# Performance work log

Hardware: AMD Instinct MI355X
Metric: run time of the kernel (lower is better)

Reference implementation:

```python
import jax, jax.numpy as jnp
import numpy as np

B, C, HH, WW, HEADS = 4, 64, 256, 256, 8
CH = C // HEADS              # 8 per-head dim
HID = int(C * 2.66)          # 170
EPS_LN = 1e-5
EPS = 1e-6
QK_NORM = 1.0
# crpe windows for 8 heads: {3:2, 5:3, 7:3}; each conv input split = head_split*Ch*2
WINDOWS = [(3, 2), (5, 3), (7, 3)]


def conv2d(x, w, b=None, groups=1, pad=0):
    out = jax.lax.conv_general_dilated(
        x, w, (1, 1), [(pad, pad), (pad, pad)],
        dimension_numbers=('NCHW', 'OIHW', 'NCHW'), feature_group_count=groups)
    return out if b is None else out + b[None, :, None, None]


def setup_inputs() -> dict:
    key = jax.random.key(0)
    ks = jax.random.split(key, 32)
    p = lambda k, shp, s=0.05: jax.random.normal(k, shp, jnp.float32) * s
    inp = {
        'x': jax.random.normal(ks[0], (B, HH * WW, C), jnp.float32),
        'ln1_w': jnp.ones((C,), jnp.float32) + p(ks[1], (C,), 0.01),
        'sca_w': p(ks[2], (C, C, 1, 1)), 'sca_b': p(ks[3], (C,)),
        'dw1_w': p(ks[4], (2 * C, C, 1, 1)),          # 1x1 dim->2dim
        'dw2_w': p(ks[5], (C, 2, 3, 3)),              # grouped 3x3, groups=C, in/grp=2
        'qkv_w': p(ks[6], (3 * C, C, 1, 1)),
        'qkv_dw_w': p(ks[7], (3 * C, 1, 3, 3)),       # depthwise 3x3
        'temperature': jnp.ones((HEADS, 1, 1), jnp.float32),
        'r3_w': p(ks[8], (2, 2 * CH, 3, 3)), 'r3_b': p(ks[9], (2,)),
        'r5_w': p(ks[10], (3, 2 * CH, 5, 5)), 'r5_b': p(ks[11], (3,)),
        'r7_w': p(ks[12], (3, 2 * CH, 7, 7)), 'r7_b': p(ks[13], (3,)),
        'proj_w': p(ks[14], (C, C, 1, 1)),
        'ln2_w': jnp.ones((C,), jnp.float32) + p(ks[15], (C,), 0.01),
        'pin_w': p(ks[16], (2 * HID, C, 1, 1)),
        'ffn_dw_w': p(ks[17], (2 * HID, 1, 3, 3)),
        'pout_w': p(ks[18], (C, HID, 1, 1)),
        'H': HH, 'W': WW,
    }
    return inp


def biasfree_ln(x, w):
    # BiasFree LayerNorm over channel dim of NCHW (var only, no mean-subtract)
    sigma = jnp.var(x, axis=1, keepdims=True)
    return x / jnp.sqrt(sigma + EPS_LN) * w[None, :, None, None]


def refine_att(q, k, H, W, convs):
    # q: (B,h,N,Ch)  k: (B,h,Ch,N) -> per-head conv relative position map (B,h,N,1)
    b, h, N, Ch = q.shape
    q_img = q.transpose(0, 1, 3, 2).reshape(b, h, Ch, H, W)
    k_img = k.reshape(b, h, Ch, H, W)
    qk = jnp.concatenate([q_img, k_img], axis=2).reshape(b, h * 2 * Ch, H, W)
    splits = np.cumsum([s * 2 * Ch for _, s in WINDOWS])[:-1]
    parts = jnp.split(qk, splits, axis=1)
    outs = [conv2d(xp, wt, bs, groups=g, pad=win // 2)
            for (win, g), (wt, bs), xp in zip(WINDOWS, convs, parts)]
    att = jnp.concatenate(outs, axis=1)           # (b, h, H, W)
    return att.reshape(b, h, 1, H * W).transpose(0, 1, 3, 2)  # (b,h,N,1)


def attention(x, sca_w, sca_b, dw1_w, dw2_w, qkv_w, qkv_dw_w, temperature,
              refine_convs, proj_w, H, W):
    b, c, _, _ = x.shape
    N = H * W
    xsca = conv2d(jnp.mean(x, axis=(2, 3), keepdims=True), sca_w, sca_b)
    x1 = conv2d(conv2d(x, dw1_w), dw2_w, groups=c, pad=1)
    qkv = conv2d(conv2d(x, qkv_w), qkv_dw_w, groups=3 * c, pad=1)
    q, k, v = jnp.split(qkv, 3, axis=1)
    q = q.reshape(b, HEADS, CH, N).transpose(0, 1, 3, 2)  # b h N Ch
    k = k.reshape(b, HEADS, CH, N)                        # b h Ch N
    v = v.reshape(b, HEADS, CH, N).transpose(0, 1, 3, 2)  # b h N Ch
    q = q / (jnp.linalg.norm(q, axis=-1, keepdims=True) / QK_NORM + EPS)
    k = k / (jnp.linalg.norm(k, axis=-2, keepdims=True) / QK_NORM + EPS)
    refine_w = jax.nn.sigmoid(refine_att(q, k, H, W, refine_convs))
    attn = k @ v                                           # b h Ch Ch
    out_num = jnp.sum(v, axis=-2, keepdims=True) + q @ attn
    ksum = jnp.sum(k, axis=-1, keepdims=True)              # b h Ch 1
    out_den = jnp.asarray(N, q.dtype) + q @ ksum + EPS     # b h N 1 (bcast to Ch)
    out = out_num / out_den * temperature
    out = out * refine_w
    out = out.transpose(0, 1, 3, 2).reshape(b, c, H, W)
    out = out * xsca * jax.nn.gelu(x1, approximate=False)
    return conv2d(out, proj_w)


def feedforward(x, pin_w, ffn_dw_w, pout_w):
    h = conv2d(x, pin_w)
    h = conv2d(h, ffn_dw_w, groups=2 * HID, pad=1)
    h1, h2 = jnp.split(h, 2, axis=1)
    return conv2d(jax.nn.gelu(h1, approximate=False) * h2, pout_w)


def reference(x, ln1_w, sca_w, sca_b, dw1_w, dw2_w, qkv_w, qkv_dw_w, temperature,
              r3_w, r3_b, r5_w, r5_b, r7_w, r7_b, proj_w, ln2_w,
              pin_w, ffn_dw_w, pout_w, H, W):
    b = x.shape[0]
    xi = x.reshape(b, H, W, C).transpose(0, 3, 1, 2)  # NCHW
    refine_convs = [(r3_w, r3_b), (r5_w, r5_b), (r7_w, r7_b)]
    xi = xi + attention(biasfree_ln(xi, ln1_w), sca_w, sca_b, dw1_w, dw2_w,
                        qkv_w, qkv_dw_w, temperature, refine_convs, proj_w, H, W)
    xi = xi + feedforward(biasfree_ln(xi, ln2_w), pin_w, ffn_dw_w, pout_w)
    return xi
```

## Files before the change

### kernel.cpp

```cpp
#include <hip/hip_runtime.h>
#include <math.h>
#include <stdio.h>

#define BB 4
#define NP 65536

typedef unsigned short u16;
typedef unsigned int u32;
typedef __attribute__((ext_vector_type(8))) short short8;
typedef __attribute__((ext_vector_type(4))) float f32x4;
typedef __attribute__((ext_vector_type(2))) float f32x2;

__device__ __forceinline__ float bf2f(u16 u) { return __uint_as_float((u32)u << 16); }
__device__ __forceinline__ u16 f2bf(float f) {
  u32 u = __float_as_uint(f);
  u = (u + 0x7FFFu + ((u >> 16) & 1u)) >> 16;
  return (u16)u;
}
__device__ __forceinline__ float gelu_f(float x) {
  return 0.5f * x * (1.f + erff(x * 0.70710678118654752f));
}
__device__ __forceinline__ float wlo(u32 w) { return __uint_as_float(w << 16); }
__device__ __forceinline__ float whi(u32 w) { return __uint_as_float(w & 0xFFFF0000u); }

__global__ __launch_bounds__(256) void k_trans_stats(const float* __restrict__ x,
                                                     float* __restrict__ xi,
                                                     u16* __restrict__ xb1,
                                                     float* __restrict__ meanraw) {
  __shared__ float tile[64 * 65];
  __shared__ float s1a[64], s2a[64], sig[64], cm[64];
  int b = blockIdx.y;
  long n0 = (long)blockIdx.x * 64;
  int t = threadIdx.x;
  for (int i = t; i < 4096; i += 256) {
    int nl = i >> 6, c = i & 63;
    tile[nl * 65 + c] = x[((long)b * NP + n0 + nl) * 64 + c];
  }
  if (t < 64) { s1a[t] = 0.f; s2a[t] = 0.f; cm[t] = 0.f; }
  __syncthreads();
  {
    int nl = t & 63, part = t >> 6;
    float p1 = 0.f, p2 = 0.f;
    for (int cc = 0; cc < 16; cc++) {
      float v = tile[nl * 65 + part * 16 + cc];
      p1 += v; p2 += v * v;
    }
    atomicAdd(&s1a[nl], p1); atomicAdd(&s2a[nl], p2);
  }
  __syncthreads();
  if (t < 64) {
    float m = s1a[t] * (1.f / 64.f);
    float var = s2a[t] * (1.f / 64.f) - m * m;
    sig[t] = rsqrtf(var + 1e-5f);
  }
  __syncthreads();
  int nl = t & 63;
  int part = t >> 6;
  float sgv = sig[nl];
  for (int j = 0; j < 16; j++) {
    int i = t + 256 * j;
    int c = i >> 6;
    float v = tile[nl * 65 + c];
    xi[((long)b * 64 + c) * NP + n0 + nl] = v;
    float a = v * sgv;
    for (int off = 32; off; off >>= 1) a += __shfl_down(a, off);
    if ((t & 63) == 0) atomicAdd(&cm[c], a);
  }
  {
    u16* rp = xb1 + ((long)b * NP + n0 + nl) * 64 + part * 16;
    uint4 pk[2];
    u32 tmp[8];
#pragma unroll
    for (int g = 0; g < 2; g++) {
#pragma unroll
      for (int e = 0; e < 4; e++) {
        float v0 = tile[nl * 65 + part * 16 + g * 8 + 2 * e] * sgv;
        float v1 = tile[nl * 65 + part * 16 + g * 8 + 2 * e + 1] * sgv;
        tmp[e] = (u32)f2bf(v0) | ((u32)f2bf(v1) << 16);
      }
      pk[g].x = tmp[0]; pk[g].y = tmp[1]; pk[g].z = tmp[2]; pk[g].w = tmp[3];
      *(uint4*)(rp + g * 8) = pk[g];
    }
  }
  __syncthreads();
  if (t < 64) atomicAdd(&meanraw[b * 64 + t], cm[t]);
}

__global__ void k_xsca(const float* __restrict__ meanraw, const float* __restrict__ lnw,
                       const float* __restrict__ sca_w, const float* __restrict__ sca_b,
                       float* __restrict__ xsca) {
  int t = threadIdx.x;
  int b = t >> 6, co = t & 63;
  float a = sca_b[co];
  for (int ci = 0; ci < 64; ci++)
    a += sca_w[co * 64 + ci] * meanraw[b * 64 + ci] * lnw[ci] * (1.f / 65536.f);
  xsca[t] = a;
}

__global__ void k_foldW1b(const float* __restrict__ qkv_w, const float* __restrict__ dw1_w,
                          const float* __restrict__ lnw, u16* __restrict__ W1b) {
  int i = blockIdx.x * 256 + threadIdx.x;
  if (i < 320 * 64) {
    int co = i >> 6, ci = i & 63;
    float w = (co < 192) ? qkv_w[co * 64 + ci] : dw1_w[(co - 192) * 64 + ci];
    W1b[i] = f2bf(w * lnw[ci]);
  }
}
__global__ void k_foldW2b(const float* __restrict__ pin_w, const float* __restrict__ lnw,
                          u16* __restrict__ W2b) {
  int i = blockIdx.x * 256 + threadIdx.x;
  if (i < 384 * 64) {
    int co = i >> 6, ci = i & 63;
    float v = 0.f;
    if (co < 340) {
      int pair = co >> 1, which = co & 1;
      v = pin_w[(pair + which * 170) * 64 + ci] * lnw[ci];
    }
    W2b[i] = f2bf(v);
  }
}
__global__ void k_foldWpb(const float* __restrict__ w, u16* __restrict__ Wpb) {
  int i = blockIdx.x * 256 + threadIdx.x;
  if (i < 4096) Wpb[i] = f2bf(w[i]);
}
__global__ void k_tpoutb(const float* __restrict__ w, u16* __restrict__ Wob) {
  int i = blockIdx.x * 256 + threadIdx.x;
  if (i < 64 * 192) {
    int co = i / 192, ci = i - co * 192;
    Wob[i] = (ci < 170) ? f2bf(w[co * 170 + ci]) : (u16)0;
  }
}

template <int EPI>
__global__ __launch_bounds__(256) void k_mgemm(const u16* __restrict__ in, long in_bs,
                                               const u16* __restrict__ W,
                                               u16* __restrict__ outp, long out_bs,
                                               float* __restrict__ xo,
                                               u16* __restrict__ xb2r) {
  int t = threadIdx.x;
  int lane = t & 63, wv = t >> 6;
  int l15 = lane & 15, quad = lane >> 4;
  int pxw = blockIdx.x * 256 + wv * 64;
  int co0 = blockIdx.y * 64;
  int b = blockIdx.z;
  const u16* inb = in + (long)b * in_bs;

  short8 aw[4][2];
#pragma unroll
  for (int t4 = 0; t4 < 4; t4++)
#pragma unroll
    for (int kf = 0; kf < 2; kf++)
      aw[t4][kf] = *(const short8*)(W + (long)(co0 + t4 * 16 + l15) * 64 + kf * 32 + quad * 8);

  f32x4 acc[4][4];
#pragma unroll
  for (int t4 = 0; t4 < 4; t4++)
#pragma unroll
    for (int p = 0; p < 4; p++) acc[t4][p] = (f32x4){0.f, 0.f, 0.f, 0.f};

#pragma unroll
  for (int p = 0; p < 4; p++) {
    long px = pxw + p * 16 + l15;
    short8 bf0 = *(const short8*)(inb + px * 64 + quad * 8);
    short8 bf1 = *(const short8*)(inb + px * 64 + 32 + quad * 8);
#pragma unroll
    for (int t4 = 0; t4 < 4; t4++) {
      acc[t4][p] = __builtin_amdgcn_mfma_f32_16x16x32_bf16(aw[t4][0], bf0, acc[t4][p], 0, 0, 0);
      acc[t4][p] = __builtin_amdgcn_mfma_f32_16x16x32_bf16(aw[t4][1], bf1, acc[t4][p], 0, 0, 0);
    }
  }

  if (EPI == 0) {
    u16* ob = outp + (long)b * out_bs;
#pragma unroll
    for (int t4 = 0; t4 < 4; t4++)
#pragma unroll
      for (int p = 0; p < 4; p++) {
#pragma unroll
        for (int reg = 0; reg < 4; reg++) {
          int co = co0 + t4 * 16 + quad * 4 + reg;
          ob[(long)co * NP + pxw + p * 16 + l15] = f2bf(acc[t4][p][reg]);
        }
      }
  } else {
#pragma unroll
    for (int p = 0; p < 4; p++) {
      long px = pxw + p * 16 + l15;
      float xv[16];
      float s1 = 0.f, s2 = 0.f;
#pragma unroll
      for (int t4 = 0; t4 < 4; t4++)
#pragma unroll
        for (int reg = 0; reg < 4; reg++) {
          int co = t4 * 16 + quad * 4 + reg;
          float v = xo[((long)b * 64 + co) * NP + px] + acc[t4][p][reg];
          xv[t4 * 4 + reg] = v;
          s1 += v; s2 += v * v;
        }
      s1 += __shfl_xor(s1, 16); s2 += __shfl_xor(s2, 16);
      s1 += __shfl_xor(s1, 32); s2 += __shfl_xor(s2, 32);
      float m = s1 * (1.f / 64.f);
      float var = s2 * (1.f / 64.f) - m * m;
      float sg = rsqrtf(var + 1e-5f);
#pragma unroll
      for (int t4 = 0; t4 < 4; t4++)
#pragma unroll
        for (int reg = 0; reg < 4; reg++) {
          int co = t4 * 16 + quad * 4 + reg;
          xo[((long)b * 64 + co) * NP + px] = xv[t4 * 4 + reg];
        }
      u16* rp = xb2r + ((long)b * NP + px) * 64;
#pragma unroll
      for (int t4 = 0; t4 < 4; t4++) {
        u32 u0 = (u32)f2bf(xv[t4 * 4 + 0] * sg) | ((u32)f2bf(xv[t4 * 4 + 1] * sg) << 16);
        u32 u1 = (u32)f2bf(xv[t4 * 4 + 2] * sg) | ((u32)f2bf(xv[t4 * 4 + 3] * sg) << 16);
        uint2 pk; pk.x = u0; pk.y = u1;
        *(uint2*)(rp + t4 * 16 + quad * 4) = pk;
      }
    }
  }
}

__device__ __forceinline__ void dw4x2(const u16* __restrict__ img, int y0, int x0, int lane,
                                      const float* __restrict__ w9,
                                      f32x2 o0[2], f32x2 o1[2]) {
  o0[0] = (f32x2){0.f, 0.f}; o0[1] = (f32x2){0.f, 0.f};
  o1[0] = (f32x2){0.f, 0.f}; o1[1] = (f32x2){0.f, 0.f};
#pragma unroll
  for (int r = -1; r <= 2; r++) {
    int row = y0 + r;
    uint2 q; q.x = 0u; q.y = 0u;
    if ((unsigned)row < 256u) q = *(const uint2*)(img + row * 256 + x0);
    u32 qly = (u32)__shfl_up((int)q.y, 1);
    u32 qrx = (u32)__shfl_down((int)q.x, 1);
    if (lane == 0)  qly = 0u;
    if (lane == 63) qrx = 0u;
    float f[6];
    f[0] = whi(qly); f[1] = wlo(q.x); f[2] = whi(q.x);
    f[3] = wlo(q.y); f[4] = whi(q.y); f[5] = wlo(qrx);
    f32x2 fp[5];
#pragma unroll
    for (int i = 0; i < 5; i++) fp[i] = (f32x2){f[i], f[i + 1]};
    if (r <= 1) {
      const float* wr = w9 + (r + 1) * 3;
#pragma unroll
      for (int dx = 0; dx < 3; dx++) {
        f32x2 w2 = {wr[dx], wr[dx]};
        o0[0] += w2 * fp[dx]; o0[1] += w2 * fp[dx + 2];
      }
    }
    if (r >= 0) {
      const float* wr = w9 + r * 3;
#pragma unroll
      for (int dx = 0; dx < 3; dx++) {
        f32x2 w2 = {wr[dx], wr[dx]};
        o1[0] += w2 * fp[dx]; o1[1] += w2 * fp[dx + 2];
      }
    }
  }
}

__global__ __launch_bounds__(256) void k_dwqkv(const u16* __restrict__ P,
                                               const float* __restrict__ dww,
                                               u16* __restrict__ Qn, u16* __restrict__ Kn,
                                               u16* __restrict__ Vn) {
  int t = threadIdx.x;
  int lane = t & 63, wv = t >> 6;
  int by = blockIdx.y;
  int ph = by >> 3, h = by & 7;
  int b = blockIdx.z;
  int y0 = (blockIdx.x * 4 + wv) * 2;
  int x0 = lane * 4;
  int cbase = ph * 64 + h * 8;
  const u16* Pb = P + ((long)b * 192 + cbase) * NP;
  const float* wb = dww + cbase * 9;

  f32x2 v[8][2][2];
#pragma unroll
  for (int c = 0; c < 8; c++)
    dw4x2(Pb + (long)c * NP, y0, x0, lane, wb + c * 9, v[c][0], v[c][1]);

  if (ph < 2) {
#pragma unroll
    for (int row = 0; row < 2; row++) {
      f32x2 s2a = {0.f, 0.f}, s2b = {0.f, 0.f};
#pragma unroll
      for (int c = 0; c < 8; c++) {
        s2a += v[c][row][0] * v[c][row][0];
        s2b += v[c][row][1] * v[c][row][1];
      }
      f32x2 ia, ib;
      ia.x = 1.f / (sqrtf(s2a.x) + 1e-6f); ia.y = 1.f / (sqrtf(s2a.y) + 1e-6f);
      ib.x = 1.f / (sqrtf(s2b.x) + 1e-6f); ib.y = 1.f / (sqrtf(s2b.y) + 1e-6f);
#pragma unroll
      for (int c = 0; c < 8; c++) { v[c][row][0] *= ia; v[c][row][1] *= ib; }
    }
  }
  u16* dst = (ph == 0) ? Qn : (ph == 1) ? Kn : Vn;
#pragma unroll
  for (int c = 0; c < 8; c++)
#pragma unroll
    for (int row = 0; row < 2; row++) {
      ushort4 st;
      st.x = f2bf(v[c][row][0].x); st.y = f2bf(v[c][row][0].y);
      st.z = f2bf(v[c][row][1].x); st.w = f2bf(v[c][row][1].y);
      *(ushort4*)(dst + ((long)b * 64 + h * 8 + c) * NP + (long)(y0 + row) * 256 + x0) = st;
    }
}

__global__ __launch_bounds__(256) void k_stats(const u16* __restrict__ Kn,
                                               const u16* __restrict__ Vn,
                                               float* __restrict__ stats) {
  int t = threadIdx.x;
  int lane = t & 63;
  int h = blockIdx.y, b = blockIdx.z;
  long px = (long)blockIdx.x * 1024 + t * 4;
  const u16* Kb = Kn + ((long)b * 64 + h * 8) * NP + px;
  const u16* Vb = Vn + ((long)b * 64 + h * 8) * NP + px;
  float kf[8][4], vf[8][4];
#pragma unroll
  for (int c = 0; c < 8; c++) {
    ushort4 ku = *(const ushort4*)(Kb + (long)c * NP);
    kf[c][0] = bf2f(ku.x); kf[c][1] = bf2f(ku.y);
    kf[c][2] = bf2f(ku.z); kf[c][3] = bf2f(ku.w);
  }
#pragma unroll
  for (int c = 0; c < 8; c++) {
    ushort4 vu = *(const ushort4*)(Vb + (long)c * NP);
    vf[c][0] = bf2f(vu.x); vf[c][1] = bf2f(vu.y);
    vf[c][2] = bf2f(vu.z); vf[c][3] = bf2f(vu.w);
  }
  __shared__ float sred[80];
  if (t < 80) sred[t] = 0.f;
  __syncthreads();
#pragma unroll
  for (int i = 0; i < 8; i++) {
#pragma unroll
    for (int j = 0; j < 8; j++) {
      float a = kf[i][0] * vf[j][0] + kf[i][1] * vf[j][1] +
                kf[i][2] * vf[j][2] + kf[i][3] * vf[j][3];
      a += __shfl_xor(a, 1); a += __shfl_xor(a, 2); a += __shfl_xor(a, 4);
      a += __shfl_xor(a, 8); a += __shfl_xor(a, 16); a += __shfl_xor(a, 32);
      if (lane == ((i * 8 + j) & 63)) atomicAdd(&sred[i * 8 + j], a);
    }
    {
      float a = kf[i][0] + kf[i][1] + kf[i][2] + kf[i][3];
      a += __shfl_xor(a, 1); a += __shfl_xor(a, 2); a += __shfl_xor(a, 4);
      a += __shfl_xor(a, 8); a += __shfl_xor(a, 16); a += __shfl_xor(a, 32);
      if (lane == ((64 + i) & 63)) atomicAdd(&sred[64 + i], a);
    }
    {
      float a = vf[i][0] + vf[i][1] + vf[i][2] + vf[i][3];
      a += __shfl_xor(a, 1); a += __shfl_xor(a, 2); a += __shfl_xor(a, 4);
      a += __shfl_xor(a, 8); a += __shfl_xor(a, 16); a += __shfl_xor(a, 32);
      if (lane == ((72 + i) & 63)) atomicAdd(&sred[72 + i], a);
    }
  }
  __syncthreads();
  if (t < 80) atomicAdd(&stats[((long)b * 8 + h) * 80 + t], sred[t]);
}

__global__ __launch_bounds__(256) void k_dwg(const u16* __restrict__ P,
                                             const float* __restrict__ dw2_w,
                                             u16* __restrict__ G) {
  int t = threadIdx.x;
  int lane = t & 63, wv = t >> 6;
  int c = blockIdx.y, b = blockIdx.z;
  int y0 = (blockIdx.x * 4 + wv) * 2;
  int x0 = lane * 4;
  const u16* Pb = P + (long)b * 128 * NP;
  f32x2 d1r0[2], d1r1[2], d2r0[2], d2r1[2];
  dw4x2(Pb + (long)(2 * c) * NP, y0, x0, lane, dw2_w + c * 18, d1r0, d1r1);
  dw4x2(Pb + (long)(2 * c + 1) * NP, y0, x0, lane, dw2_w + c * 18 + 9, d2r0, d2r1);
  u16* gp = G + ((long)b * 64 + c) * NP + (long)y0 * 256 + x0;
  ushort4 s0, s1;
  s0.x = f2bf(gelu_f(d1r0[0].x + d2r0[0].x)); s0.y = f2bf(gelu_f(d1r0[0].y + d2r0[0].y));
  s0.z = f2bf(gelu_f(d1r0[1].x + d2r0[1].x)); s0.w = f2bf(gelu_f(d1r0[1].y + d2r0[1].y));
  s1.x = f2bf(gelu_f(d1r1[0].x + d2r1[0].x)); s1.y = f2bf(gelu_f(d1r1[0].y + d2r1[0].y));
  s1.z = f2bf(gelu_f(d1r1[1].x + d2r1[1].x)); s1.w = f2bf(gelu_f(d1r1[1].y + d2r1[1].y));
  *(ushort4*)(gp) = s0;
  *(ushort4*)(gp + 256) = s1;
}

__global__ __launch_bounds__(256) void k_dwgate(const u16* __restrict__ P,
                                                const float* __restrict__ dww,
                                                u16* __restrict__ Hb) {
  int t = threadIdx.x;
  int lane = t & 63, wv = t >> 6;
  int c = blockIdx.y, b = blockIdx.z;
  int y0 = (blockIdx.x * 4 + wv) * 2;
  int x0 = lane * 4;
  const u16* Pb = P + (long)b * 384 * NP;
  f32x2 d1r0[2], d1r1[2], d2r0[2], d2r1[2];
  dw4x2(Pb + (long)(2 * c) * NP, y0, x0, lane, dww + c * 9, d1r0, d1r1);
  dw4x2(Pb + (long)(2 * c + 1) * NP, y0, x0, lane, dww + (170 + c) * 9, d2r0, d2r1);
  u16* hp = Hb + ((long)b * 170 + c) * NP + (long)y0 * 256 + x0;
  ushort4 s0, s1;
  s0.x = f2bf(gelu_f(d1r0[0].x) * d2r0[0].x); s0.y = f2bf(gelu_f(d1r0[0].y) * d2r0[0].y);
  s0.z = f2bf(gelu_f(d1r0[1].x) * d2r0[1].x); s0.w = f2bf(gelu_f(d1r0[1].y) * d2r0[1].y);
  s1.x = f2bf(gelu_f(d1r1[0].x) * d2r1[0].x); s1.y = f2bf(gelu_f(d1r1[0].y) * d2r1[0].y);
  s1.z = f2bf(gelu_f(d1r1[1].x) * d2r1[1].x); s1.w = f2bf(gelu_f(d1r1[1].y) * d2r1[1].y);
  *(ushort4*)(hp) = s0;
  *(ushort4*)(hp + 256) = s1;
}

template <int WIN>
__device__ void refine1(const u16* __restrict__ src, const float* __restrict__ wp,
                        float bias, float* __restrict__ ro, int y0, int x0, int lane) {
  const int R = WIN / 2;
  f32x2 a0a = {bias, bias}, a0b = {bias, bias};
  f32x2 a1a = {bias, bias}, a1b = {bias, bias};
#pragma unroll 1
  for (int ch = 0; ch < 8; ch++) {
    const u16* img = src + (long)ch * NP;
    const float* wc = wp + ch * WIN * WIN;
#pragma unroll
    for (int r = -R; r <= 1 + R; r++) {
      int row = y0 + r;
      uint2 q; q.x = 0u; q.y = 0u;
      if ((unsigned)row < 256u) q = *(const uint2*)(img + row * 256 + x0);
      float f[4 + 2 * R];
      f[R + 0] = wlo(q.x); f[R + 1] = whi(q.x);
      f[R + 2] = wlo(q.y); f[R + 3] = whi(q.y);
      {
        u32 qly = (u32)__shfl_up((int)q.y, 1);
        u32 qrx = (u32)__shfl_down((int)q.x, 1);
        if (lane == 0)  qly = 0u;
        if (lane == 63) qrx = 0u;
        f[R - 1] = whi(qly); f[R + 4] = wlo(qrx);
        if (R >= 2) { f[R - 2] = wlo(qly); f[R + 5] = whi(qrx); }
        if (R >= 3) {
          u32 qlx = (u32)__shfl_up((int)q.x, 1);
          u32 qry = (u32)__shfl_down((int)q.y, 1);
          if (lane == 0)  qlx = 0u;
          if (lane == 63) qry = 0u;
          f[0] = whi(qlx); f[R + 6] = wlo(qry);
        }
      }
      f32x2 fp[3 + 2 * R];
#pragma unroll
      for (int i = 0; i < 3 + 2 * R; i++) fp[i] = (f32x2){f[i], f[i + 1]};
      if (r <= R) {
        const float* w0 = wc + (r + R) * WIN;
#pragma unroll
        for (int dx = 0; dx < WIN; dx++) {
          f32x2 w2 = {w0[dx], w0[dx]};
          a0a += w2 * fp[dx];
          a0b += w2 * fp[dx + 2];
        }
      }
      if (r >= 1 - R) {
        const float* w1 = wc + (r - 1 + R) * WIN;
#pragma unroll
        for (int dx = 0; dx < WIN; dx++) {
          f32x2 w2 = {w1[dx], w1[dx]};
          a1a += w2 * fp[dx];
          a1b += w2 * fp[dx + 2];
        }
      }
    }
  }
  float4 o0, o1;
  o0.x = a0a.x; o0.y = a0a.y; o0.z = a0b.x; o0.w = a0b.y;
  o1.x = a1a.x; o1.y = a1a.y; o1.z = a1b.x; o1.w = a1b.y;
  *(float4*)(ro + (long)y0 * 256 + x0) = o0;
  *(float4*)(ro + (long)(y0 + 1) * 256 + x0) = o1;
}

__global__ __launch_bounds__(256) void k_refine(
    const u16* __restrict__ Qn, const u16* __restrict__ Kn,
    const float* __restrict__ r3w, const float* __restrict__ r3b,
    const float* __restrict__ r5w, const float* __restrict__ r5b,
    const float* __restrict__ r7w, const float* __restrict__ r7b,
    float* __restrict__ refQ, float* __restrict__ refK) {
  int t = threadIdx.x, lane = t & 63, wv = t >> 6;
  int yy = blockIdx.y;
  int h = ((yy >> 1) + 5) & 7;
  int ph = yy & 1;
  int b = blockIdx.z;
  int y0 = (blockIdx.x * 4 + wv) * 2;
  int x0 = lane * 4;
  const u16* src = (ph ? Kn : Qn) + ((long)b * 64 + h * 8) * NP;
  float* ro = (ph ? refK : refQ) + ((long)(b * 8 + h)) * NP;
  if (h < 2) {
    float bias = ph ? 0.f : r3b[h];
    refine1<3>(src, r3w + h * 16 * 9 + ph * 8 * 9, bias, ro, y0, x0, lane);
  } else if (h < 5) {
    float bias = ph ? 0.f : r5b[h - 2];
    refine1<5>(src, r5w + (h - 2) * 16 * 25 + ph * 8 * 25, bias, ro, y0, x0, lane);
  } else {
    float bias = ph ? 0.f : r7b[h - 5];
    refine1<7>(src, r7w + (h - 5) * 16 * 49 + ph * 8 * 49, bias, ro, y0, x0, lane);
  }
}

__global__ __launch_bounds__(256) void k_attn(
    const u16* __restrict__ Qn, const float* __restrict__ stats,
    const float* __restrict__ refQ, const float* __restrict__ refK,
    const float* __restrict__ temp,
    const float* __restrict__ xsca, const u16* __restrict__ G,
    u16* __restrict__ Orows) {
  int b = blockIdx.y;
  int t = threadIdx.x;
  __shared__ float s[640];
  __shared__ float sx[64];
  for (int i = t; i < 640; i += 256) s[i] = stats[(long)b * 640 + i];
  if (t < 64) sx[t] = xsca[b * 64 + t];
  __syncthreads();
  long n = (long)blockIdx.x * 256 + t;
  u16* rp = Orows + ((long)b * NP + n) * 64;
#pragma unroll
  for (int h = 0; h < 8; h++) {
    const float* sh = s + h * 80;
    float q[8];
#pragma unroll
    for (int i = 0; i < 8; i++) q[i] = bf2f(Qn[((long)b * 64 + h * 8 + i) * NP + n]);
    float den = 65536.f + 1e-6f;
#pragma unroll
    for (int i = 0; i < 8; i++) den += q[i] * sh[64 + i];
    float rsum = refQ[((long)(b * 8 + h)) * NP + n] + refK[((long)(b * 8 + h)) * NP + n];
    float tr = temp[h] / ((1.f + expf(-rsum)) * den);
    u32 pk[4];
#pragma unroll
    for (int j2 = 0; j2 < 4; j2++) {
      float o01[2];
#pragma unroll
      for (int e = 0; e < 2; e++) {
        int j = j2 * 2 + e;
        float num = sh[72 + j];
#pragma unroll
        for (int i = 0; i < 8; i++) num += q[i] * sh[i * 8 + j];
        int ci = h * 8 + j;
        o01[e] = num * tr * sx[ci] * bf2f(G[((long)b * 64 + ci) * NP + n]);
      }
      pk[j2] = (u32)f2bf(o01[0]) | ((u32)f2bf(o01[1]) << 16);
    }
    uint4 v; v.x = pk[0]; v.y = pk[1]; v.z = pk[2]; v.w = pk[3];
    *(uint4*)(rp + h * 8) = v;
  }
}

__global__ __launch_bounds__(256) void k_pout(const u16* __restrict__ Hb,
                                              const u16* __restrict__ Wob,
                                              float* __restrict__ xo) {
  __shared__ u16 tile[64 * 196];
  int t = threadIdx.x;
  int lane = t & 63, wv = t >> 6;
  int l15 = lane & 15, quad = lane >> 4;
  int b = blockIdx.z;
  int px0 = blockIdx.x * 64;
  const u16* ib = Hb + (long)b * 170 * NP + px0;
#pragma unroll
  for (int i = 0; i < 12; i++) {
    int task = t + i * 256;
    int q = task >> 6, px = task & 63;
    int ci0 = q * 4;
    u32 w0 = 0u, w1 = 0u;
    if (ci0 < 170)     w0 = (u32)ib[(long)ci0 * NP + px];
    if (ci0 + 1 < 170) w0 |= ((u32)ib[(long)(ci0 + 1) * NP + px]) << 16;
    if (ci0 + 2 < 170) w1 = (u32)ib[(long)(ci0 + 2) * NP + px];
    if (ci0 + 3 < 170) w1 |= ((u32)ib[(long)(ci0 + 3) * NP + px]) << 16;
    uint2 pk; pk.x = w0; pk.y = w1;
    *(uint2*)(tile + px * 196 + ci0) = pk;
  }
  __syncthreads();

  f32x4 acc[4];
#pragma unroll
  for (int t4 = 0; t4 < 4; t4++) acc[t4] = (f32x4){0.f, 0.f, 0.f, 0.f};
  const u16* tb = tile + (wv * 16 + l15) * 196;
#pragma unroll
  for (int kf = 0; kf < 6; kf++) {
    union { uint2 u2[2]; short8 s8; } cv;
    cv.u2[0] = *(const uint2*)(tb + kf * 32 + quad * 8);
    cv.u2[1] = *(const uint2*)(tb + kf * 32 + quad * 8 + 4);
    short8 bfr = cv.s8;
#pragma unroll
    for (int t4 = 0; t4 < 4; t4++) {
      short8 aw = *(const short8*)(Wob + (long)(t4 * 16 + l15) * 192 + kf * 32 + quad * 8);
      acc[t4] = __builtin_amdgcn_mfma_f32_16x16x32_bf16(aw, bfr, acc[t4], 0, 0, 0);
    }
  }
  long pxg = px0 + wv * 16 + l15;
  float* xb = xo + (long)b * 64 * NP;
#pragma unroll
  for (int t4 = 0; t4 < 4; t4++)
#pragma unroll
    for (int reg = 0; reg < 4; reg++) {
      int co = t4 * 16 + quad * 4 + reg;
      xb[(long)co * NP + pxg] += acc[t4][reg];
    }
}

extern "C" void kernel_launch(void* const* d_in, const int* in_sizes, int n_in,
                              void* d_out, int out_size, void* d_ws, size_t ws_size,
                              hipStream_t stream) {
  const float* x        = (const float*)d_in[0];
  const float* ln1_w    = (const float*)d_in[1];
  const float* sca_w    = (const float*)d_in[2];
  const float* sca_b    = (const float*)d_in[3];
  const float* dw1_w    = (const float*)d_in[4];
  const float* dw2_w    = (const float*)d_in[5];
  const float* qkv_w    = (const float*)d_in[6];
  const float* qkv_dw_w = (const float*)d_in[7];
  const float* temp     = (const float*)d_in[8];
  const float* r3w = (const float*)d_in[9],  *r3b = (const float*)d_in[10];
  const float* r5w = (const float*)d_in[11], *r5b = (const float*)d_in[12];
  const float* r7w = (const float*)d_in[13], *r7b = (const float*)d_in[14];
  const float* proj_w   = (const float*)d_in[15];
  const float* ln2_w    = (const float*)d_in[16];
  const float* pin_w    = (const float*)d_in[17];
  const float* ffn_dw_w = (const float*)d_in[18];
  const float* pout_w   = (const float*)d_in[19];
  float* out = (float*)d_out;
  char* wsb = (char*)d_ws;

  const size_t Mi = 1048576;
  u16* xb1   = (u16*)(wsb);
  u16* Qn    = (u16*)(wsb + 32 * Mi);
  u16* Kn    = (u16*)(wsb + 64 * Mi);
  u16* G     = (u16*)(wsb + 96 * Mi);
  u16* Preg  = (u16*)(wsb + 128 * Mi);
  float* refQ    = (float*)(wsb + 224 * Mi);
  float* refK    = (float*)(wsb + 128 * Mi);
  float* Fm      = (float*)(wsb + 232 * Mi);
  float* stats   = Fm;
  float* meanraw = Fm + 2560;
  float* xscab   = Fm + 2816;
  u16* Wob       = (u16*)(Fm + 3072);
  u16* W1b = (u16*)(Fm + 13952);
  u16* W2b = W1b + 20480;
  u16* Wpb = W2b + 24576;
  u16* xb2 = xb1;
  u16* Orows = Kn;
  u16* Hb = Qn;
  u16* Vn = G;

  const size_t needed = 232 * Mi + 13952 * 4 + (20480 + 24576 + 4096) * 2;
  if (ws_size < needed) {
    fprintf(stderr, "kernel_launch: ws_size %zu < needed %zu\n", ws_size, needed);
    return;
  }

  hipMemsetAsync(stats, 0, (2560 + 256) * 4, stream);
  k_foldW1b<<<80, 256, 0, stream>>>(qkv_w, dw1_w, ln1_w, W1b);
  k_foldW2b<<<96, 256, 0, stream>>>(pin_w, ln2_w, W2b);
  k_foldWpb<<<16, 256, 0, stream>>>(proj_w, Wpb);
  k_tpoutb<<<48, 256, 0, stream>>>(pout_w, Wob);

  k_trans_stats<<<dim3(1024, BB), 256, 0, stream>>>(x, out, xb1, meanraw);
  k_xsca<<<1, 256, 0, stream>>>(meanraw, ln1_w, sca_w, sca_b, xscab);

  k_mgemm<0><<<dim3(256, 3, BB), 256, 0, stream>>>(xb1, (long)NP * 64, W1b,
                                                   Preg, 192L * NP, nullptr, nullptr);
  k_dwqkv<<<dim3(32, 24, BB), 256, 0, stream>>>(Preg, qkv_dw_w, Qn, Kn, Vn);
  k_stats<<<dim3(64, 8, BB), 256, 0, stream>>>(Kn, Vn, stats);

  k_mgemm<0><<<dim3(256, 2, BB), 256, 0, stream>>>(xb1, (long)NP * 64, W1b + 192 * 64,
                                                   Preg, 128L * NP, nullptr, nullptr);
  k_dwg<<<dim3(32, 64, BB), 256, 0, stream>>>(Preg, dw2_w, G);

  k_refine<<<dim3(32, 16, BB), 256, 0, stream>>>(Qn, Kn, r3w, r3b, r5w, r5b, r7w, r7b,
                                                 refQ, refK);
  k_attn<<<dim3(256, BB), 256, 0, stream>>>(Qn, stats, refQ, refK, temp, xscab, G, Orows);

  k_mgemm<1><<<dim3(256, 1, BB), 256, 0, stream>>>(Orows, (long)NP * 64, Wpb,
                                                   nullptr, 0, out, xb2);

  for (int pass = 0; pass < 2; pass++) {
    k_mgemm<0><<<dim3(256, 6, 2), 256, 0, stream>>>(xb2 + (long)pass * 2 * NP * 64,
                                                    (long)NP * 64, W2b,
                                                    Preg, 384L * NP, nullptr, nullptr);
    k_dwgate<<<dim3(32, 170, 2), 256, 0, stream>>>(Preg, ffn_dw_w,
                                                   Hb + (long)pass * 2 * 170 * NP);
  }
  k_pout<<<dim3(1024, 1, BB), 256, 0, stream>>>(Hb, Wob, out);
}
```

Before: 852.8 us.

## Drop NCHW residual copy and read residual from original NHWC input in projection epilogue

The first LayerNorm kernel no longer stages a tile in shared memory or writes a transposed fp32 copy of x into the output buffer. It computes per-pixel statistics with wave shuffles on float4 loads and writes only the bf16 normalized rows plus channel means. The projection GEMM epilogue now reads the residual directly from the original x in pixel-major layout with vector loads instead of strided NCHW reads. This removes a full fp32 write and changes the residual read pattern; the output buffer is still written in NCHW by the epilogue.

```diff
diff --git a/kernel.cpp b/kernel.cpp
--- a/kernel.cpp
+++ b/kernel.cpp
@@ -23,64 +23,47 @@
 __device__ __forceinline__ float wlo(u32 w) { return __uint_as_float(w << 16); }
 __device__ __forceinline__ float whi(u32 w) { return __uint_as_float(w & 0xFFFF0000u); }
 
-__global__ __launch_bounds__(256) void k_trans_stats(const float* __restrict__ x,
-                                                     float* __restrict__ xi,
-                                                     u16* __restrict__ xb1,
-                                                     float* __restrict__ meanraw) {
-  __shared__ float tile[64 * 65];
-  __shared__ float s1a[64], s2a[64], sig[64], cm[64];
+__global__ __launch_bounds__(256) void k_ln1(const float* __restrict__ x,
+                                             u16* __restrict__ xb1,
+                                             float* __restrict__ meanraw) {
+  int t = threadIdx.x;
   int b = blockIdx.y;
-  long n0 = (long)blockIdx.x * 64;
-  int t = threadIdx.x;
-  for (int i = t; i < 4096; i += 256) {
-    int nl = i >> 6, c = i & 63;
-    tile[nl * 65 + c] = x[((long)b * NP + n0 + nl) * 64 + c];
-  }
-  if (t < 64) { s1a[t] = 0.f; s2a[t] = 0.f; cm[t] = 0.f; }
+  int lane = t & 63;
+  int cg = t & 15;
+  float a0 = 0.f, a1 = 0.f, a2 = 0.f, a3 = 0.f;
+#pragma unroll
+  for (int it = 0; it < 8; it++) {
+    long px = (long)blockIdx.x * 128 + (t >> 4) + it * 16;
+    const float* xr = x + ((long)b * NP + px) * 64 + cg * 4;
+    float4 v = *(const float4*)(xr);
+    float s1 = v.x + v.y + v.z + v.w;
+    float s2 = v.x * v.x + v.y * v.y + v.z * v.z + v.w * v.w;
+    s1 += __shfl_xor(s1, 1); s2 += __shfl_xor(s2, 1);
+    s1 += __shfl_xor(s1, 2); s2 += __shfl_xor(s2, 2);
+    s1 += __shfl_xor(s1, 4); s2 += __shfl_xor(s2, 4);
+    s1 += __shfl_xor(s1, 8); s2 += __shfl_xor(s2, 8);
+    float m = s1 * (1.f / 64.f);
+    float var = s2 * (1.f / 64.f) - m * m;
+    float sg = rsqrtf(var + 1e-5f);
+    float h0 = v.x * sg, h1 = v.y * sg, h2 = v.z * sg, h3 = v.w * sg;
+    uint2 pk;
+    pk.x = (u32)f2bf(h0) | ((u32)f2bf(h1) << 16);
+    pk.y = (u32)f2bf(h2) | ((u32)f2bf(h3) << 16);
+    *(uint2*)(xb1 + ((long)b * NP + px) * 64 + cg * 4) = pk;
+    a0 += h0; a1 += h1; a2 += h2; a3 += h3;
+  }
+  a0 += __shfl_xor(a0, 16); a1 += __shfl_xor(a1, 16);
+  a2 += __shfl_xor(a2, 16); a3 += __shfl_xor(a3, 16);
+  a0 += __shfl_xor(a0, 32); a1 += __shfl_xor(a1, 32);
+  a2 += __shfl_xor(a2, 32); a3 += __shfl_xor(a3, 32);
+  __shared__ float cm[64];
+  if (t < 64) cm[t] = 0.f;
   __syncthreads();
-  {
-    int nl = t & 63, part = t >> 6;
-    float p1 = 0.f, p2 = 0.f;
-    for (int cc = 0; cc < 16; cc++) {
-      float v = tile[nl * 65 + part * 16 + cc];
-      p1 += v; p2 += v * v;
-    }
-    atomicAdd(&s1a[nl], p1); atomicAdd(&s2a[nl], p2);
-  }
-  __syncthreads();
-  if (t < 64) {
-    float m = s1a[t] * (1.f / 64.f);
-    float var = s2a[t] * (1.f / 64.f) - m * m;
-    sig[t] = rsqrtf(var + 1e-5f);
-  }
-  __syncthreads();
-  int nl = t & 63;
-  int part = t >> 6;
-  float sgv = sig[nl];
-  for (int j = 0; j < 16; j++) {
-    int i = t + 256 * j;
-    int c = i >> 6;
-    float v = tile[nl * 65 + c];
-    xi[((long)b * 64 + c) * NP + n0 + nl] = v;
-    float a = v * sgv;
-    for (int off = 32; off; off >>= 1) a += __shfl_down(a, off);
-    if ((t & 63) == 0) atomicAdd(&cm[c], a);
-  }
-  {
-    u16* rp = xb1 + ((long)b * NP + n0 + nl) * 64 + part * 16;
-    uint4 pk[2];
-    u32 tmp[8];
-#pragma unroll
-    for (int g = 0; g < 2; g++) {
-#pragma unroll
-      for (int e = 0; e < 4; e++) {
-        float v0 = tile[nl * 65 + part * 16 + g * 8 + 2 * e] * sgv;
-        float v1 = tile[nl * 65 + part * 16 + g * 8 + 2 * e + 1] * sgv;
-        tmp[e] = (u32)f2bf(v0) | ((u32)f2bf(v1) << 16);
-      }
-      pk[g].x = tmp[0]; pk[g].y = tmp[1]; pk[g].z = tmp[2]; pk[g].w = tmp[3];
-      *(uint4*)(rp + g * 8) = pk[g];
-    }
+  if (lane < 16) {
+    atomicAdd(&cm[cg * 4 + 0], a0);
+    atomicAdd(&cm[cg * 4 + 1], a1);
+    atomicAdd(&cm[cg * 4 + 2], a2);
+    atomicAdd(&cm[cg * 4 + 3], a3);
   }
   __syncthreads();
   if (t < 64) atomicAdd(&meanraw[b * 64 + t], cm[t]);
@@ -135,6 +118,7 @@
 __global__ __launch_bounds__(256) void k_mgemm(const u16* __restrict__ in, long in_bs,
                                                const u16* __restrict__ W,
                                                u16* __restrict__ outp, long out_bs,
+                                               const float* __restrict__ xres,
                                                float* __restrict__ xo,
                                                u16* __restrict__ xb2r) {
   int t = threadIdx.x;
@@ -186,14 +170,18 @@
 #pragma unroll
     for (int p = 0; p < 4; p++) {
       long px = pxw + p * 16 + l15;
+      const float* xrow = xres + ((long)b * NP + px) * 64;
+      f32x4 xr[4];
+#pragma unroll
+      for (int t4 = 0; t4 < 4; t4++)
+        xr[t4] = *(const f32x4*)(xrow + t4 * 16 + quad * 4);
       float xv[16];
       float s1 = 0.f, s2 = 0.f;
 #pragma unroll
       for (int t4 = 0; t4 < 4; t4++)
 #pragma unroll
         for (int reg = 0; reg < 4; reg++) {
-          int co = t4 * 16 + quad * 4 + reg;
-          float v = xo[((long)b * 64 + co) * NP + px] + acc[t4][p][reg];
+          float v = xr[t4][reg] + acc[t4][p][reg];
           xv[t4 * 4 + reg] = v;
           s1 += v; s2 += v * v;
         }
@@ -648,16 +636,16 @@
   k_foldWpb<<<16, 256, 0, stream>>>(proj_w, Wpb);
   k_tpoutb<<<48, 256, 0, stream>>>(pout_w, Wob);
 
-  k_trans_stats<<<dim3(1024, BB), 256, 0, stream>>>(x, out, xb1, meanraw);
+  k_ln1<<<dim3(512, BB), 256, 0, stream>>>(x, xb1, meanraw);
   k_xsca<<<1, 256, 0, stream>>>(meanraw, ln1_w, sca_w, sca_b, xscab);
 
   k_mgemm<0><<<dim3(256, 3, BB), 256, 0, stream>>>(xb1, (long)NP * 64, W1b,
-                                                   Preg, 192L * NP, nullptr, nullptr);
+                                                   Preg, 192L * NP, nullptr, nullptr, nullptr);
   k_dwqkv<<<dim3(32, 24, BB), 256, 0, stream>>>(Preg, qkv_dw_w, Qn, Kn, Vn);
   k_stats<<<dim3(64, 8, BB), 256, 0, stream>>>(Kn, Vn, stats);
 
   k_mgemm<0><<<dim3(256, 2, BB), 256, 0, stream>>>(xb1, (long)NP * 64, W1b + 192 * 64,
-                                                   Preg, 128L * NP, nullptr, nullptr);
+                                                   Preg, 128L * NP, nullptr, nullptr, nullptr);
   k_dwg<<<dim3(32, 64, BB), 256, 0, stream>>>(Preg, dw2_w, G);
 
   k_refine<<<dim3(32, 16, BB), 256, 0, stream>>>(Qn, Kn, r3w, r3b, r5w, r5b, r7w, r7b,
@@ -665,12 +653,12 @@
   k_attn<<<dim3(256, BB), 256, 0, stream>>>(Qn, stats, refQ, refK, temp, xscab, G, Orows);
 
   k_mgemm<1><<<dim3(256, 1, BB), 256, 0, stream>>>(Orows, (long)NP * 64, Wpb,
-                                                   nullptr, 0, out, xb2);
+                                                   nullptr, 0, x, out, xb2);
 
   for (int pass = 0; pass < 2; pass++) {
     k_mgemm<0><<<dim3(256, 6, 2), 256, 0, stream>>>(xb2 + (long)pass * 2 * NP * 64,
                                                     (long)NP * 64, W2b,
-                                                    Preg, 384L * NP, nullptr, nullptr);
+                                                    Preg, 384L * NP, nullptr, nullptr, nullptr);
     k_dwgate<<<dim3(32, 170, 2), 256, 0, stream>>>(Preg, ffn_dw_w,
                                                    Hb + (long)pass * 2 * 170 * NP);
   }
```

Result: faster. 723.3 us (-15.2%).
